# Kernel optimization log

Hardware: AMD Instinct MI355X
Metric: run time of the kernel (lower is better)

Reference implementation:

```python
import jax, jax.numpy as jnp
import numpy as np

EPS = 1e-08
STEPS_START = 0
STEPS_END = 500


def setup_inputs() -> dict:
    key = jax.random.key(0)
    k_x, k_w, k_beta, k_b = jax.random.split(key, 4)
    B, T, D_in, D_out = 64, 500, 1024, 128
    x = jax.random.normal(k_x, (B, T, D_in), dtype=jnp.float32)
    # w ~ N(w_init_mean, w_init_std * sqrt(1/input_shape))
    w = jax.random.normal(k_w, (D_in, D_out), dtype=jnp.float32) * np.sqrt(1.0 / D_in)
    beta = jax.random.uniform(k_beta, (D_out,), dtype=jnp.float32)  # clamped to [0,1] in torch
    b = jax.random.uniform(k_b, (D_out,), dtype=jnp.float32)        # clamped >= 0 in torch
    return {"x": x, "w": w, "beta": beta, "b": b}


def reference(x, w, beta, b):
    # x: [B, T, D_in], w: [D_in, D_out], beta/b: [D_out]
    h = jnp.einsum('btc,cd->btd', x, w)          # [B, T, D_out]
    norm = jnp.sum(w * w, axis=0)                # [D_out]

    one_minus_beta = 1.0 - beta

    def step(mem, h_t):
        mem = mem * beta + one_minus_beta * h_t  # Leaky_Neuron=True
        return mem, mem

    mem0 = jnp.zeros((x.shape[0], w.shape[1]), dtype=x.dtype)
    _, mem_rec = jax.lax.scan(step, mem0, jnp.swapaxes(h, 0, 1))  # [T, B, D_out]
    mem_rec = jnp.swapaxes(mem_rec, 0, 1)                          # [B, T, D_out]

    # time_reduction == 'mean'
    output = jnp.mean(mem_rec[:, STEPS_START:STEPS_END, :], axis=1) / (norm + EPS) - b
    return output
```

## Files before the change

kernel.cpp:

```cpp
#include <hip/hip_runtime.h>
#include <hip/hip_bf16.h>

#define B_    64
#define T_    500
#define DIN   1024
#define DOUT  128
#define EPSV  1e-8f
#define BM    128
#define BK    64
#define NKC   2
#define KCL   (DIN / NKC)
#define NKT   (KCL / BK)
#define TILES 4

typedef __attribute__((ext_vector_type(8))) short bf16x8;
typedef __attribute__((ext_vector_type(4))) float f32x4;

#define OFF_WTAB  262144
#define OFF_SCALE 518144
#define OFF_PART  518656

__device__ inline short f2bf(float f) {
    __hip_bfloat16 h = __float2bfloat16(f);
    return __builtin_bit_cast(short, h);
}

__global__ __launch_bounds__(256) void prep_kernel(
    const float* __restrict__ w, const float* __restrict__ beta,
    __hip_bfloat16* __restrict__ wT, float* __restrict__ wtab,
    float* __restrict__ scale)
{
    int bid = blockIdx.x, tid = threadIdx.x;
    if (bid < 512) {
        int i = bid * 256 + tid;
        int d = i >> 10, k = i & 1023;
        wT[(size_t)d * DIN + k] = __float2bfloat16(w[(size_t)k * DOUT + d]);
    } else if (bid < 640) {
        int d = bid - 512;
        __shared__ float red[256];
        float s = 0.f;
        for (int c = tid; c < DIN; c += 256) {
            float v = w[(size_t)c * DOUT + d];
            s += v * v;
        }
        red[tid] = s;
        __syncthreads();
        for (int off = 128; off > 0; off >>= 1) {
            if (tid < off) red[tid] += red[tid + off];
            __syncthreads();
        }
        if (tid == 0) scale[d] = 1.f / ((red[0] + EPSV) * (float)T_);
    } else {
        int i = (bid - 640) * 256 + tid;
        if (i < T_ * DOUT) {
            int t = i >> 7, d = i & 127;
            wtab[i] = 1.f - powf(beta[d], (float)(T_ - t));
        }
    }
}

__global__ __launch_bounds__(512, 4) void gemm_kernel(
    const float* __restrict__ x, const __hip_bfloat16* __restrict__ wT,
    const float* __restrict__ wtab, float* __restrict__ partials)
{
    __shared__ __align__(16) char smem[2 * 32768];

    const int wg   = blockIdx.x;
    const int kc   = wg & 1;
    const int tile = (wg >> 1) & 3;
    const int b    = wg >> 3;
    const int t0   = tile * BM;
    const int kbase = kc * KCL;
    const int tid  = threadIdx.x;
    const int wid  = tid >> 6;
    const int lane = tid & 63;
    const int arow = lane & 15;
    const int kblk = lane >> 4;
    const int wr   = wid >> 2;
    const int wc   = wid & 3;

    const float* xb = x + (size_t)b * T_ * DIN + kbase;

    const int sr = tid >> 4;
    const int sc = tid & 15;
    const float* ag[4];
    int awoff[4];
#pragma unroll
    for (int p = 0; p < 4; ++p) {
        int row  = p * 32 + sr;
        int trow = t0 + row; if (trow >= T_) trow = T_ - 1;
        ag[p] = xb + (size_t)trow * DIN + sc * 4;
        awoff[p] = (row * 128 + sc * 8) ^ ((row & 7) << 4);
    }
    const int bcol = tid >> 2;
    const int bch0 = (tid & 3) * 2;
    const __hip_bfloat16* bg0 = wT + (size_t)bcol * DIN + kbase + bch0 * 8;
    const __hip_bfloat16* bg1 = bg0 + 8;
    const int bwoff0 = (bcol * 128 + bch0 * 16)        ^ ((bcol & 7) << 4);
    const int bwoff1 = (bcol * 128 + (bch0 + 1) * 16)  ^ ((bcol & 7) << 4);

    int aro[4][2], bro[2][2];
#pragma unroll
    for (int fm = 0; fm < 4; ++fm)
#pragma unroll
        for (int kk = 0; kk < 2; ++kk) {
            int row = wr * 64 + fm * 16 + arow;
            aro[fm][kk] = (row * 128 + kk * 64 + kblk * 16) ^ ((row & 7) << 4);
        }
#pragma unroll
    for (int fn = 0; fn < 2; ++fn)
#pragma unroll
        for (int kk = 0; kk < 2; ++kk) {
            int col = wc * 32 + fn * 16 + arow;
            bro[fn][kk] = (col * 128 + kk * 64 + kblk * 16) ^ ((col & 7) << 4);
        }

    f32x4 acc[4][2] = {};

    {
        char* Ab = smem;
        char* Bb = smem + 16384;
#pragma unroll
        for (int p = 0; p < 4; ++p) {
            float4 v = *reinterpret_cast<const float4*>(ag[p]);
            short4 h; h.x = f2bf(v.x); h.y = f2bf(v.y); h.z = f2bf(v.z); h.w = f2bf(v.w);
            *reinterpret_cast<short4*>(Ab + awoff[p]) = h;
        }
        *reinterpret_cast<bf16x8*>(Bb + bwoff0) = *reinterpret_cast<const bf16x8*>(bg0);
        *reinterpret_cast<bf16x8*>(Bb + bwoff1) = *reinterpret_cast<const bf16x8*>(bg1);
    }
    __syncthreads();

    for (int kt = 0; kt < NKT; ++kt) {
        const int cur = kt & 1;
        char* Acur = smem + cur * 32768;
        char* Bcur = Acur + 16384;
        char* Anxt = smem + (cur ^ 1) * 32768;
        char* Bnxt = Anxt + 16384;

        float4 av[4]; bf16x8 bv0, bv1;
        if (kt < NKT - 1) {
            const int kb = (kt + 1) * BK;
#pragma unroll
            for (int p = 0; p < 4; ++p)
                av[p] = *reinterpret_cast<const float4*>(ag[p] + kb);
            bv0 = *reinterpret_cast<const bf16x8*>(bg0 + kb);
            bv1 = *reinterpret_cast<const bf16x8*>(bg1 + kb);
        }

#pragma unroll
        for (int kk = 0; kk < 2; ++kk) {
            bf16x8 bf0 = *reinterpret_cast<const bf16x8*>(Bcur + bro[0][kk]);
            bf16x8 bf1 = *reinterpret_cast<const bf16x8*>(Bcur + bro[1][kk]);
#pragma unroll
            for (int fm = 0; fm < 4; ++fm) {
                bf16x8 af = *reinterpret_cast<const bf16x8*>(Acur + aro[fm][kk]);
                acc[fm][0] = __builtin_amdgcn_mfma_f32_16x16x32_bf16(af, bf0, acc[fm][0], 0, 0, 0);
                acc[fm][1] = __builtin_amdgcn_mfma_f32_16x16x32_bf16(af, bf1, acc[fm][1], 0, 0, 0);
            }
        }

        if (kt < NKT - 1) {
#pragma unroll
            for (int p = 0; p < 4; ++p) {
                short4 h; h.x = f2bf(av[p].x); h.y = f2bf(av[p].y);
                h.z = f2bf(av[p].z); h.w = f2bf(av[p].w);
                *reinterpret_cast<short4*>(Anxt + awoff[p]) = h;
            }
            *reinterpret_cast<bf16x8*>(Bnxt + bwoff0) = bv0;
            *reinterpret_cast<bf16x8*>(Bnxt + bwoff1) = bv1;
        }
        __syncthreads();
    }

    const int col0 = wc * 32 + arow;
    const int col1 = col0 + 16;
    float s0 = 0.f, s1 = 0.f;
#pragma unroll
    for (int fm = 0; fm < 4; ++fm) {
#pragma unroll
        for (int r = 0; r < 4; ++r) {
            int t = t0 + wr * 64 + fm * 16 + kblk * 4 + r;
            if (t < T_) {
                s0 += wtab[t * DOUT + col0] * acc[fm][0][r];
                s1 += wtab[t * DOUT + col1] * acc[fm][1][r];
            }
        }
    }
    s0 += __shfl_xor(s0, 16); s0 += __shfl_xor(s0, 32);
    s1 += __shfl_xor(s1, 16); s1 += __shfl_xor(s1, 32);

    if (kblk == 0) {
        float* p = partials + ((((size_t)b * TILES + tile) * 2 + wr) * NKC + kc) * DOUT;
        p[col0] = s0;
        p[col1] = s1;
    }
}

__global__ __launch_bounds__(256) void finalize_kernel(
    const float* __restrict__ partials, const float* __restrict__ scale,
    const float* __restrict__ bias, float* __restrict__ out)
{
    int i = blockIdx.x * 256 + threadIdx.x;
    int b = i >> 7, d = i & 127;
    float s = 0.f;
#pragma unroll
    for (int p = 0; p < TILES * 2 * NKC; ++p)
        s += partials[((size_t)b * TILES * 2 * NKC + p) * DOUT + d];
    out[i] = s * scale[d] - bias[d];
}

extern "C" void kernel_launch(void* const* d_in, const int* in_sizes, int n_in,
                              void* d_out, int out_size, void* d_ws, size_t ws_size,
                              hipStream_t stream) {
    const float* x    = (const float*)d_in[0];
    const float* w    = (const float*)d_in[1];
    const float* beta = (const float*)d_in[2];
    const float* bias = (const float*)d_in[3];
    float* out = (float*)d_out;

    char* ws = (char*)d_ws;
    __hip_bfloat16* wT = (__hip_bfloat16*)(ws);
    float* wtab     = (float*)(ws + OFF_WTAB);
    float* scale    = (float*)(ws + OFF_SCALE);
    float* partials = (float*)(ws + OFF_PART);

    prep_kernel<<<890, 256, 0, stream>>>(w, beta, wT, wtab, scale);
    gemm_kernel<<<B_ * TILES * NKC, 512, 0, stream>>>(x, wT, wtab, partials);
    finalize_kernel<<<(B_ * DOUT) / 256, 256, 0, stream>>>(partials, scale, bias, out);
}
```

Baseline: 36.87 us.

## Prefetch global tiles two stages ahead with register double-buffering and lighter barriers

New measurement: 34.66 us. 1.06x faster.

```diff
diff --git a/kernel.cpp b/kernel.cpp
--- a/kernel.cpp
+++ b/kernel.cpp
@@ -23,6 +23,12 @@
 __device__ inline short f2bf(float f) {
     __hip_bfloat16 h = __float2bfloat16(f);
     return __builtin_bit_cast(short, h);
+}
+
+__device__ inline void block_sync_lds() {
+    asm volatile("s_waitcnt lgkmcnt(0)" ::: "memory");
+    __builtin_amdgcn_s_barrier();
+    asm volatile("" ::: "memory");
 }
 
 __global__ __launch_bounds__(256) void prep_kernel(
@@ -117,61 +123,69 @@
 
     f32x4 acc[4][2] = {};
 
-    {
-        char* Ab = smem;
-        char* Bb = smem + 16384;
-#pragma unroll
-        for (int p = 0; p < 4; ++p) {
-            float4 v = *reinterpret_cast<const float4*>(ag[p]);
-            short4 h; h.x = f2bf(v.x); h.y = f2bf(v.y); h.z = f2bf(v.z); h.w = f2bf(v.w);
-            *reinterpret_cast<short4*>(Ab + awoff[p]) = h;
-        }
-        *reinterpret_cast<bf16x8*>(Bb + bwoff0) = *reinterpret_cast<const bf16x8*>(bg0);
-        *reinterpret_cast<bf16x8*>(Bb + bwoff1) = *reinterpret_cast<const bf16x8*>(bg1);
-    }
-    __syncthreads();
-
+#define DECL_SET(S) float4 S##a0, S##a1, S##a2, S##a3; bf16x8 S##b0, S##b1;
+#define LOAD_SET(S, KB) \
+    S##a0 = *reinterpret_cast<const float4*>(ag[0] + (KB)); \
+    S##a1 = *reinterpret_cast<const float4*>(ag[1] + (KB)); \
+    S##a2 = *reinterpret_cast<const float4*>(ag[2] + (KB)); \
+    S##a3 = *reinterpret_cast<const float4*>(ag[3] + (KB)); \
+    S##b0 = *reinterpret_cast<const bf16x8*>(bg0 + (KB));   \
+    S##b1 = *reinterpret_cast<const bf16x8*>(bg1 + (KB));
+#define WRITE_SET(S, AB, BB) { \
+    short4 h0; h0.x=f2bf(S##a0.x); h0.y=f2bf(S##a0.y); h0.z=f2bf(S##a0.z); h0.w=f2bf(S##a0.w); \
+    *reinterpret_cast<short4*>((AB) + awoff[0]) = h0; \
+    short4 h1; h1.x=f2bf(S##a1.x); h1.y=f2bf(S##a1.y); h1.z=f2bf(S##a1.z); h1.w=f2bf(S##a1.w); \
+    *reinterpret_cast<short4*>((AB) + awoff[1]) = h1; \
+    short4 h2; h2.x=f2bf(S##a2.x); h2.y=f2bf(S##a2.y); h2.z=f2bf(S##a2.z); h2.w=f2bf(S##a2.w); \
+    *reinterpret_cast<short4*>((AB) + awoff[2]) = h2; \
+    short4 h3; h3.x=f2bf(S##a3.x); h3.y=f2bf(S##a3.y); h3.z=f2bf(S##a3.z); h3.w=f2bf(S##a3.w); \
+    *reinterpret_cast<short4*>((AB) + awoff[3]) = h3; \
+    *reinterpret_cast<bf16x8*>((BB) + bwoff0) = S##b0; \
+    *reinterpret_cast<bf16x8*>((BB) + bwoff1) = S##b1; }
+#define COMPUTE(AB, BB) { \
+    _Pragma("unroll") \
+    for (int kk = 0; kk < 2; ++kk) { \
+        bf16x8 bf0 = *reinterpret_cast<const bf16x8*>((BB) + bro[0][kk]); \
+        bf16x8 bf1 = *reinterpret_cast<const bf16x8*>((BB) + bro[1][kk]); \
+        _Pragma("unroll") \
+        for (int fm = 0; fm < 4; ++fm) { \
+            bf16x8 af = *reinterpret_cast<const bf16x8*>((AB) + aro[fm][kk]); \
+            acc[fm][0] = __builtin_amdgcn_mfma_f32_16x16x32_bf16(af, bf0, acc[fm][0], 0, 0, 0); \
+            acc[fm][1] = __builtin_amdgcn_mfma_f32_16x16x32_bf16(af, bf1, acc[fm][1], 0, 0, 0); \
+        } } }
+
+    DECL_SET(qe_)
+    DECL_SET(qo_)
+
+    LOAD_SET(qe_, 0)
+    LOAD_SET(qo_, BK)
+    WRITE_SET(qe_, smem, smem + 16384)
+    block_sync_lds();
+
+#pragma unroll
     for (int kt = 0; kt < NKT; ++kt) {
-        const int cur = kt & 1;
-        char* Acur = smem + cur * 32768;
+        char* Acur = smem + (kt & 1) * 32768;
         char* Bcur = Acur + 16384;
-        char* Anxt = smem + (cur ^ 1) * 32768;
+        char* Anxt = smem + ((kt + 1) & 1) * 32768;
         char* Bnxt = Anxt + 16384;
 
-        float4 av[4]; bf16x8 bv0, bv1;
-        if (kt < NKT - 1) {
-            const int kb = (kt + 1) * BK;
-#pragma unroll
-            for (int p = 0; p < 4; ++p)
-                av[p] = *reinterpret_cast<const float4*>(ag[p] + kb);
-            bv0 = *reinterpret_cast<const bf16x8*>(bg0 + kb);
-            bv1 = *reinterpret_cast<const bf16x8*>(bg1 + kb);
-        }
-
-#pragma unroll
-        for (int kk = 0; kk < 2; ++kk) {
-            bf16x8 bf0 = *reinterpret_cast<const bf16x8*>(Bcur + bro[0][kk]);
-            bf16x8 bf1 = *reinterpret_cast<const bf16x8*>(Bcur + bro[1][kk]);
-#pragma unroll
-            for (int fm = 0; fm < 4; ++fm) {
-                bf16x8 af = *reinterpret_cast<const bf16x8*>(Acur + aro[fm][kk]);
-                acc[fm][0] = __builtin_amdgcn_mfma_f32_16x16x32_bf16(af, bf0, acc[fm][0], 0, 0, 0);
-                acc[fm][1] = __builtin_amdgcn_mfma_f32_16x16x32_bf16(af, bf1, acc[fm][1], 0, 0, 0);
-            }
-        }
-
-        if (kt < NKT - 1) {
-#pragma unroll
-            for (int p = 0; p < 4; ++p) {
-                short4 h; h.x = f2bf(av[p].x); h.y = f2bf(av[p].y);
-                h.z = f2bf(av[p].z); h.w = f2bf(av[p].w);
-                *reinterpret_cast<short4*>(Anxt + awoff[p]) = h;
-            }
-            *reinterpret_cast<bf16x8*>(Bnxt + bwoff0) = bv0;
-            *reinterpret_cast<bf16x8*>(Bnxt + bwoff1) = bv1;
-        }
-        __syncthreads();
-    }
+        if (kt + 2 < NKT) {
+            if (kt & 1) { LOAD_SET(qo_, (kt + 2) * BK) }
+            else        { LOAD_SET(qe_, (kt + 2) * BK) }
+        }
+
+        COMPUTE(Acur, Bcur)
+
+        if (kt + 1 < NKT) {
+            if (kt & 1) { WRITE_SET(qe_, Anxt, Bnxt) }
+            else        { WRITE_SET(qo_, Anxt, Bnxt) }
+            block_sync_lds();
+        }
+    }
+#undef DECL_SET
+#undef LOAD_SET
+#undef WRITE_SET
+#undef COMPUTE
 
     const int col0 = wc * 32 + arow;
     const int col1 = col0 + 16;
```
